# Kernel optimization log

Hardware: AMD Instinct MI355X
Metric: run time of the kernel (lower is better)

## Reference

```python
import jax, jax.numpy as jnp
import numpy as np

N_NODES = 100000

def _gcn_conv(x, W, b, src, dst, ew, num_nodes):
    # x: [N, Fin], W: [Fin, Fout], src/dst: [Etot], ew: [Etot]
    xw = x @ W                                   # [N, Fout]
    deg = jax.ops.segment_sum(ew, dst, num_segments=num_nodes)   # [N]
    dinv = jnp.where(deg > 0, jax.lax.rsqrt(jnp.where(deg > 0, deg, 1.0)), 0.0)
    norm = dinv[src] * ew * dinv[dst]            # [Etot]
    msg = xw[src] * norm[:, None]                # [Etot, Fout] gather-transform
    out = jax.ops.segment_sum(msg, dst, num_segments=num_nodes)  # scatter-add
    return out + b

def setup_inputs() -> dict:
    key = jax.random.key(0)
    k1, k2, k3, k4, k5, k6, k7 = jax.random.split(key, 7)
    N, E, F_IN, HID, CLS = N_NODES, 1600000, 128, 64, 32
    x = jax.random.normal(k1, (N, F_IN), dtype=jnp.float32)
    edge_index = jax.random.randint(k2, (2, E), 0, N, dtype=jnp.int64)
    edge_weight = jax.random.uniform(k3, (E,), dtype=jnp.float32)
    s1 = 1.0 / np.sqrt(F_IN)
    s2 = 1.0 / np.sqrt(HID)
    W1 = jax.random.uniform(k4, (F_IN, HID), dtype=jnp.float32, minval=-s1, maxval=s1)
    b1 = jnp.zeros((HID,), dtype=jnp.float32)
    W2 = jax.random.uniform(k5, (HID, CLS), dtype=jnp.float32, minval=-s2, maxval=s2)
    b2 = jnp.zeros((CLS,), dtype=jnp.float32)
    return {"x": x, "edge_index": edge_index, "edge_weight": edge_weight,
            "W1": W1, "b1": b1, "W2": W2, "b2": b2}

def reference(x, edge_index, edge_weight, W1, b1, W2, b2):
    N = x.shape[0]
    # add self-loops with weight 1 (PyG GCNConv default)
    loop = jnp.arange(N, dtype=edge_index.dtype)
    src = jnp.concatenate([edge_index[0], loop])
    dst = jnp.concatenate([edge_index[1], loop])
    ew = jnp.concatenate([edge_weight, jnp.ones((N,), dtype=edge_weight.dtype)])
    h = _gcn_conv(x, W1, b1, src, dst, ew, N)
    h = jax.nn.relu(h)
    # dropout is identity in eval mode
    out = _gcn_conv(h, W2, b2, src, dst, ew, N)
    return out
```

## Files before the change

### kernel.cpp

```cpp
#include <hip/hip_runtime.h>

#define FIN 128
#define HID 64
#define CLS 32

#define BSH 7
#define BNODES 128
#define GB 1024
#define BCAP 4096

using bfrag = __attribute__((ext_vector_type(8))) short;
using cfrag = __attribute__((ext_vector_type(4))) float;

__device__ inline unsigned short f2bf(float x) {
  unsigned u = __float_as_uint(x);
  return (unsigned short)((u + 0x7FFFu + ((u >> 16) & 1u)) >> 16);
}
__device__ inline void bf8_to_f32(int4 v, float* f) {
  f[0] = __uint_as_float((unsigned)v.x << 16);
  f[1] = __uint_as_float((unsigned)v.x & 0xFFFF0000u);
  f[2] = __uint_as_float((unsigned)v.y << 16);
  f[3] = __uint_as_float((unsigned)v.y & 0xFFFF0000u);
  f[4] = __uint_as_float((unsigned)v.z << 16);
  f[5] = __uint_as_float((unsigned)v.z & 0xFFFF0000u);
  f[6] = __uint_as_float((unsigned)v.w << 16);
  f[7] = __uint_as_float((unsigned)v.w & 0xFFFF0000u);
}

__global__ __launch_bounds__(256) void k_wpack(const float* __restrict__ W1,
                                               const float* __restrict__ W2,
                                               unsigned short* __restrict__ wp1,
                                               unsigned short* __restrict__ wp2) {
  int t = blockIdx.x * 256 + threadIdx.x;
  int total = gridDim.x * 256;
  for (int i = t; i < 16 * 512; i += total) {
    int f = i >> 9, l = (i >> 3) & 63, j = i & 7;
    int ks = f >> 2, nt = f & 3;
    int k = ks * 32 + (l >> 4) * 8 + j;
    int n = nt * 16 + (l & 15);
    wp1[i] = f2bf(W1[k * 64 + n]);
  }
  for (int i = t; i < 4 * 512; i += total) {
    int f = i >> 9, l = (i >> 3) & 63, j = i & 7;
    int ks = f >> 1, nt = f & 1;
    int k = ks * 32 + (l >> 4) * 8 + j;
    int n = nt * 16 + (l & 15);
    wp2[i] = f2bf(W2[k * 32 + n]);
  }
}

__global__ __launch_bounds__(256) void k_a1(const int* __restrict__ dst,
                                            int* __restrict__ gcntT,
                                            int E, int CHUNK, int NBUK) {
  __shared__ int cnt[1024];
  for (int i = threadIdx.x; i < NBUK; i += 256) cnt[i] = 0;
  __syncthreads();
  int s = blockIdx.x * CHUNK, e = min(E, s + CHUNK);
  for (int p = s + threadIdx.x; p < e; p += 256)
    atomicAdd(&cnt[dst[p] >> BSH], 1);
  __syncthreads();
  for (int i = threadIdx.x; i < NBUK; i += 256)
    gcntT[i * GB + blockIdx.x] = cnt[i];
}

__global__ __launch_bounds__(256) void k_scan_sums(const int* __restrict__ counts,
                                                   int* __restrict__ bsum, int N) {
  __shared__ int s[256];
  int base = blockIdx.x * 4096 + threadIdx.x * 16;
  int t = 0;
#pragma unroll
  for (int j = 0; j < 16; ++j)
    if (base + j < N) t += counts[base + j];
  s[threadIdx.x] = t;
  __syncthreads();
  for (int off = 128; off > 0; off >>= 1) {
    if (threadIdx.x < off) s[threadIdx.x] += s[threadIdx.x + off];
    __syncthreads();
  }
  if (threadIdx.x == 0) bsum[blockIdx.x] = s[0];
}

__global__ __launch_bounds__(256) void k_scan_bsums(int* __restrict__ bsum, int nb) {
  __shared__ int s[256];
  int t = threadIdx.x;
  int v = (t < nb) ? bsum[t] : 0;
  s[t] = v;
  __syncthreads();
  for (int off = 1; off < 256; off <<= 1) {
    int u = (t >= off) ? s[t - off] : 0;
    __syncthreads();
    s[t] += u;
    __syncthreads();
  }
  if (t < nb) bsum[t] = s[t] - v;
}

__global__ __launch_bounds__(256) void k_scan_emit(const int* __restrict__ counts,
                                                   const int* __restrict__ bsum,
                                                   int* __restrict__ rowstart, int N) {
  __shared__ int s[256];
  int base = blockIdx.x * 4096 + threadIdx.x * 16;
  int c[16];
  int tsum = 0;
#pragma unroll
  for (int j = 0; j < 16; ++j) {
    c[j] = (base + j < N) ? counts[base + j] : 0;
    tsum += c[j];
  }
  s[threadIdx.x] = tsum;
  __syncthreads();
  for (int off = 1; off < 256; off <<= 1) {
    int v = (threadIdx.x >= off) ? s[threadIdx.x - off] : 0;
    __syncthreads();
    s[threadIdx.x] += v;
    __syncthreads();
  }
  int run = bsum[blockIdx.x] + s[threadIdx.x] - tsum;
#pragma unroll
  for (int j = 0; j < 16; ++j) {
    if (base + j < N) rowstart[base + j] = run;
    run += c[j];
  }
}

__global__ __launch_bounds__(256) void k_a2(const int* __restrict__ src,
                                            const int* __restrict__ dst,
                                            const float* __restrict__ ew,
                                            const int* __restrict__ goff,
                                            int2* __restrict__ recs,
                                            int E, int CHUNK, int NBUK) {
  __shared__ int cur[1024];
  for (int i = threadIdx.x; i < NBUK; i += 256)
    cur[i] = goff[i * GB + blockIdx.x];
  __syncthreads();
  int s = blockIdx.x * CHUNK, e = min(E, s + CHUNK);
  for (int p = s + threadIdx.x; p < e; p += 256) {
    int d = dst[p];
    int b = d >> BSH;
    int pos = atomicAdd(&cur[b], 1);
    recs[pos] = make_int2(src[p] | ((d & (BNODES - 1)) << 17), __float_as_int(ew[p]));
  }
}

__global__ __launch_bounds__(256) void k_bucket(int2* __restrict__ recs,
                                                const int* __restrict__ goff,
                                                float* __restrict__ dinv,
                                                int* __restrict__ rowstart,
                                                int N, int E, int NBUK) {
  __shared__ int2 lrec[BCAP];
  __shared__ int cnt[BNODES];
  __shared__ int cur[BNODES];
  __shared__ int sbuf[BNODES];
  __shared__ float degs[BNODES];
  __shared__ float dl[BNODES];
  const int b = blockIdx.x;
  const int t = threadIdx.x;
  const int bstart = goff[b * GB];
  const int bend = (b + 1 < NBUK) ? goff[(b + 1) * GB] : E;
  int m = bend - bstart;
  if (m > BCAP) m = BCAP;

  if (t < BNODES) { cnt[t] = 0; degs[t] = 1.0f; }
  __syncthreads();
  for (int p = t; p < m; p += 256) {
    int2 r = recs[bstart + p];
    lrec[p] = r;
    int d = (r.x >> 17) & (BNODES - 1);
    atomicAdd(&cnt[d], 1);
    atomicAdd(&degs[d], __int_as_float(r.y));
  }
  __syncthreads();
  if (t < BNODES) sbuf[t] = cnt[t];
  __syncthreads();
  for (int off = 1; off < BNODES; off <<= 1) {
    int v = (t < BNODES && t >= off) ? sbuf[t - off] : 0;
    __syncthreads();
    if (t < BNODES) sbuf[t] += v;
    __syncthreads();
  }
  if (t < BNODES) {
    int ls = sbuf[t] - cnt[t];
    cur[t] = ls;
    float di = rsqrtf(degs[t]);
    dl[t] = di;
    int node = b * BNODES + t;
    if (node < N) { dinv[node] = di; rowstart[node] = bstart + ls; }
  }
  __syncthreads();
  for (int p = t; p < m; p += 256) {
    int2 r = lrec[p];
    int d = (r.x >> 17) & (BNODES - 1);
    int pos = atomicAdd(&cur[d], 1);
    float c = __int_as_float(r.y) * dl[d];
    recs[bstart + pos] = make_int2(r.x & 0x1FFFF, __float_as_int(c));
  }
}

template <int K, int F, bool RELU>
__global__ __launch_bounds__(256, 4) void mfma_gemm(const float* __restrict__ x,
                                                    const unsigned short* __restrict__ wp,
                                                    const float* __restrict__ scale,
                                                    unsigned short* __restrict__ y, int N) {
  constexpr int KS = K / 32;
  constexpr int NT = F / 16;
  const int lane = threadIdx.x & 63;
  const int quad = lane >> 4;
  const int col = lane & 15;
  const int row0 = blockIdx.x * 64 + (threadIdx.x >> 6) * 16;
  if (row0 >= N) return;

  bfrag bf[KS * NT];
#pragma unroll
  for (int f = 0; f < KS * NT; ++f)
    bf[f] = *(const bfrag*)(wp + f * 512 + lane * 8);

  cfrag acc[NT] = {};

  int row_a = row0 + col;
  if (row_a >= N) row_a = N - 1;
  const float* xp = x + (size_t)row_a * K + quad * 8;

#pragma unroll
  for (int ks = 0; ks < KS; ++ks) {
    float4 a0 = *(const float4*)(xp + ks * 32);
    float4 a1 = *(const float4*)(xp + ks * 32 + 4);
    if (RELU) {
      a0.x = fmaxf(a0.x, 0.f); a0.y = fmaxf(a0.y, 0.f);
      a0.z = fmaxf(a0.z, 0.f); a0.w = fmaxf(a0.w, 0.f);
      a1.x = fmaxf(a1.x, 0.f); a1.y = fmaxf(a1.y, 0.f);
      a1.z = fmaxf(a1.z, 0.f); a1.w = fmaxf(a1.w, 0.f);
    }
    bfrag af;
    af[0] = (short)f2bf(a0.x); af[1] = (short)f2bf(a0.y);
    af[2] = (short)f2bf(a0.z); af[3] = (short)f2bf(a0.w);
    af[4] = (short)f2bf(a1.x); af[5] = (short)f2bf(a1.y);
    af[6] = (short)f2bf(a1.z); af[7] = (short)f2bf(a1.w);
#pragma unroll
    for (int nt = 0; nt < NT; ++nt)
      acc[nt] = __builtin_amdgcn_mfma_f32_16x16x32_bf16(af, bf[ks * NT + nt], acc[nt], 0, 0, 0);
  }

  float scr[4];
#pragma unroll
  for (int r = 0; r < 4; ++r) {
    int row = row0 + quad * 4 + r;
    scr[r] = (row < N) ? scale[row] : 0.f;
  }
#pragma unroll
  for (int nt = 0; nt < NT; ++nt)
#pragma unroll
    for (int r = 0; r < 4; ++r) {
      int row = row0 + quad * 4 + r;
      if (row < N)
        y[(size_t)row * F + nt * 16 + col] = f2bf(scr[r] * acc[nt][r]);
    }
}

template <int F>
__global__ __launch_bounds__(256) void pull_agg(const unsigned short* __restrict__ xs,
                                                const int2* __restrict__ pairs,
                                                const int* __restrict__ rowstart,
                                                const float* __restrict__ dinv,
                                                const float* __restrict__ b,
                                                float* __restrict__ out, int N, int E) {
  constexpr int LPN = F / 8;
  constexpr int NPB = 256 / LPN;
  const int g = blockIdx.x * NPB + threadIdx.x / LPN;
  const int f8 = (threadIdx.x % LPN) * 8;
  if (g >= N) return;

  const int start = rowstart[g];
  const int end = (g + 1 < N) ? rowstart[g + 1] : E;
  const float di = dinv[g];

  float acc[8];
  {
    int4 v = *(const int4*)&xs[(size_t)g * F + f8];
    float xf[8];
    bf8_to_f32(v, xf);
    float4 b0 = *(const float4*)&b[f8];
    float4 b1 = *(const float4*)&b[f8 + 4];
    acc[0] = fmaf(di, xf[0], b0.x); acc[1] = fmaf(di, xf[1], b0.y);
    acc[2] = fmaf(di, xf[2], b0.z); acc[3] = fmaf(di, xf[3], b0.w);
    acc[4] = fmaf(di, xf[4], b1.x); acc[5] = fmaf(di, xf[5], b1.y);
    acc[6] = fmaf(di, xf[6], b1.z); acc[7] = fmaf(di, xf[7], b1.w);
  }

  int p = start;
  for (; p + 2 <= end; p += 2) {
    int2 p0 = pairs[p];
    int2 p1 = pairs[p + 1];
    int4 v0 = *(const int4*)&xs[(size_t)p0.x * F + f8];
    int4 v1 = *(const int4*)&xs[(size_t)p1.x * F + f8];
    float c0 = __int_as_float(p0.y), c1 = __int_as_float(p1.y);
    float x0[8], x1[8];
    bf8_to_f32(v0, x0);
    bf8_to_f32(v1, x1);
#pragma unroll
    for (int j = 0; j < 8; ++j) acc[j] = fmaf(c0, x0[j], acc[j]);
#pragma unroll
    for (int j = 0; j < 8; ++j) acc[j] = fmaf(c1, x1[j], acc[j]);
  }
  if (p < end) {
    int2 pa = pairs[p];
    int4 va = *(const int4*)&xs[(size_t)pa.x * F + f8];
    float ca = __int_as_float(pa.y);
    float xa[8];
    bf8_to_f32(va, xa);
#pragma unroll
    for (int j = 0; j < 8; ++j) acc[j] = fmaf(ca, xa[j], acc[j]);
  }
  *(float4*)&out[(size_t)g * F + f8] = make_float4(acc[0], acc[1], acc[2], acc[3]);
  *(float4*)&out[(size_t)g * F + f8 + 4] = make_float4(acc[4], acc[5], acc[6], acc[7]);
}

extern "C" void kernel_launch(void* const* d_in, const int* in_sizes, int n_in,
                              void* d_out, int out_size, void* d_ws, size_t ws_size,
                              hipStream_t stream) {
  const float* x  = (const float*)d_in[0];
  const int*   ei = (const int*)d_in[1];
  const float* ew = (const float*)d_in[2];
  const float* W1 = (const float*)d_in[3];
  const float* b1 = (const float*)d_in[4];
  const float* W2 = (const float*)d_in[5];
  const float* b2 = (const float*)d_in[6];
  float* out = (float*)d_out;

  const int N = in_sizes[0] / FIN;
  const int E = in_sizes[2];
  const int* src = ei;
  const int* dst = ei + E;

  const int NBUK = (N + BNODES - 1) >> BSH;
  const int M = NBUK * GB;
  const int CHUNK = (E + GB - 1) / GB;
  const int nbM = (M + 4095) / 4096;

  float* wsf      = (float*)d_ws;
  float* dinv     = wsf;
  int*   rowstart = (int*)(dinv + N);
  int*   gcntT    = rowstart + N;
  int*   bsum     = gcntT + M;
  int2*  recs     = (int2*)(bsum + 256);
  unsigned short* xs1 = (unsigned short*)(recs + E);
  float* out1     = (float*)(xs1 + (size_t)N * HID);
  unsigned short* xs2 = xs1;
  unsigned short* wp1 = (unsigned short*)(out1 + (size_t)N * HID);
  unsigned short* wp2 = wp1 + 16 * 512;

  k_wpack<<<32, 256, 0, stream>>>(W1, W2, wp1, wp2);
  k_a1<<<GB, 256, 0, stream>>>(dst, gcntT, E, CHUNK, NBUK);
  k_scan_sums<<<nbM, 256, 0, stream>>>(gcntT, bsum, M);
  k_scan_bsums<<<1, 256, 0, stream>>>(bsum, nbM);
  k_scan_emit<<<nbM, 256, 0, stream>>>(gcntT, bsum, gcntT, M);
  k_a2<<<GB, 256, 0, stream>>>(src, dst, ew, gcntT, recs, E, CHUNK, NBUK);
  k_bucket<<<NBUK, 256, 0, stream>>>(recs, gcntT, dinv, rowstart, N, E, NBUK);

  mfma_gemm<FIN, HID, false><<<(N + 63) / 64, 256, 0, stream>>>(x, wp1, dinv, xs1, N);
  pull_agg<HID><<<(N + 31) / 32, 256, 0, stream>>>(xs1, recs, rowstart, dinv, b1, out1, N, E);

  mfma_gemm<HID, CLS, true><<<(N + 63) / 64, 256, 0, stream>>>(out1, wp2, dinv, xs2, N);
  pull_agg<CLS><<<(N + 63) / 64, 256, 0, stream>>>(xs2, recs, rowstart, dinv, b2, out, N, E);
}
```

Baseline: 260.6 us.

## Stage edge records in LDS per block before coalesced bucket scatter

The record-scatter kernel now counts each bucket locally, prefix-scans the counts and writes records into a shared-memory staging buffer grouped by bucket. It then copies the staged records out in order, so consecutive threads write mostly contiguous runs of global memory instead of fully random positions. The grid block count GB drops from 1024 to 256, so each block handles a larger chunk (up to SCAP records). This adds an extra pass over dst, several barriers and about 70KB of LDS per block, which lowers occupancy. The serial per-bucket p2b fill loop may also be imbalanced.

```diff
diff --git a/kernel.cpp b/kernel.cpp
--- a/kernel.cpp
+++ b/kernel.cpp
@@ -6,8 +6,9 @@
 
 #define BSH 7
 #define BNODES 128
-#define GB 1024
+#define GB 256
 #define BCAP 4096
+#define SCAP 6272
 
 using bfrag = __attribute__((ext_vector_type(8))) short;
 using cfrag = __attribute__((ext_vector_type(4))) float;
@@ -129,16 +130,65 @@
                                             const int* __restrict__ goff,
                                             int2* __restrict__ recs,
                                             int E, int CHUNK, int NBUK) {
-  __shared__ int cur[1024];
-  for (int i = threadIdx.x; i < NBUK; i += 256)
-    cur[i] = goff[i * GB + blockIdx.x];
-  __syncthreads();
-  int s = blockIdx.x * CHUNK, e = min(E, s + CHUNK);
-  for (int p = s + threadIdx.x; p < e; p += 256) {
+  __shared__ int2 stage[SCAP];
+  __shared__ unsigned short p2b[SCAP];
+  __shared__ int lcnt[1024];
+  __shared__ int loff[1024];
+  __shared__ int lcur[1024];
+  __shared__ int gstart[1024];
+  __shared__ int ssum[256];
+  const int b = blockIdx.x, t = threadIdx.x;
+  const int s = b * CHUNK, e = min(E, s + CHUNK);
+  const int m = e - s;
+
+  for (int i = t; i < NBUK; i += 256) {
+    lcnt[i] = 0;
+    gstart[i] = goff[i * GB + b];
+  }
+  __syncthreads();
+  for (int p = s + t; p < e; p += 256)
+    atomicAdd(&lcnt[dst[p] >> BSH], 1);
+  __syncthreads();
+
+  int c[4];
+  int base = t * 4;
+  int tsum = 0;
+#pragma unroll
+  for (int j = 0; j < 4; ++j) {
+    c[j] = (base + j < NBUK) ? lcnt[base + j] : 0;
+    tsum += c[j];
+  }
+  ssum[t] = tsum;
+  __syncthreads();
+  for (int off = 1; off < 256; off <<= 1) {
+    int v = (t >= off) ? ssum[t - off] : 0;
+    __syncthreads();
+    ssum[t] += v;
+    __syncthreads();
+  }
+  int run = ssum[t] - tsum;
+#pragma unroll
+  for (int j = 0; j < 4; ++j) {
+    if (base + j < NBUK) { loff[base + j] = run; lcur[base + j] = run; }
+    run += c[j];
+  }
+  __syncthreads();
+
+  for (int i = t; i < NBUK; i += 256) {
+    int st = loff[i], en = st + lcnt[i];
+    for (int p = st; p < en; ++p) p2b[p] = (unsigned short)i;
+  }
+  for (int p = s + t; p < e; p += 256) {
     int d = dst[p];
-    int b = d >> BSH;
-    int pos = atomicAdd(&cur[b], 1);
-    recs[pos] = make_int2(src[p] | ((d & (BNODES - 1)) << 17), __float_as_int(ew[p]));
+    int bk = d >> BSH;
+    int pos = atomicAdd(&lcur[bk], 1);
+    stage[pos] = make_int2(src[p] | ((d & (BNODES - 1)) << 17), __float_as_int(ew[p]));
+  }
+  __syncthreads();
+
+  for (int p = t; p < m; p += 256) {
+    int bk = p2b[p];
+    recs[gstart[bk] + (p - loff[bk])] = stage[p];
   }
 }
 
```

New measurement: 254.6 us. 2.3% less time.

## Locally sort edge chunks in LDS before bucket scatter, staging output in shared

Applied to the files above, without the earlier changes.

Replaces the count pass plus global random scatter with a per-chunk LDS counting sort. It writes chunk-sorted records contiguously, along with per-chunk bucket offsets. The bucket kernel then gathers each bucket's contiguous segments from every chunk and writes the final CSR pairs coalesced from shared memory. This is meant to replace scattered global writes with coalesced ones and to read dst only within one kernel, at the cost of more LDS, an extra edge-sized buffer, and serial per-thread segment copies.

```diff
diff --git a/kernel.cpp b/kernel.cpp
--- a/kernel.cpp
+++ b/kernel.cpp
@@ -6,8 +6,10 @@
 
 #define BSH 7
 #define BNODES 128
-#define GB 1024
+#define GB 256
 #define BCAP 4096
+#define SCAP 6272
+#define NBUKP 800
 
 using bfrag = __attribute__((ext_vector_type(8))) short;
 using cfrag = __attribute__((ext_vector_type(4))) float;
@@ -49,18 +51,52 @@
   }
 }
 
-__global__ __launch_bounds__(256) void k_a1(const int* __restrict__ dst,
-                                            int* __restrict__ gcntT,
-                                            int E, int CHUNK, int NBUK) {
-  __shared__ int cnt[1024];
-  for (int i = threadIdx.x; i < NBUK; i += 256) cnt[i] = 0;
-  __syncthreads();
-  int s = blockIdx.x * CHUNK, e = min(E, s + CHUNK);
-  for (int p = s + threadIdx.x; p < e; p += 256)
-    atomicAdd(&cnt[dst[p] >> BSH], 1);
-  __syncthreads();
-  for (int i = threadIdx.x; i < NBUK; i += 256)
-    gcntT[i * GB + blockIdx.x] = cnt[i];
+__global__ __launch_bounds__(1024) void k_sortchunk(const int* __restrict__ src,
+                                                    const int* __restrict__ dst,
+                                                    const float* __restrict__ ew,
+                                                    int2* __restrict__ recsA,
+                                                    int* __restrict__ gcntT,
+                                                    int* __restrict__ loffB,
+                                                    int E, int CHUNK, int NBUK) {
+  __shared__ int2 stage[SCAP];
+  __shared__ int lcnt[NBUKP];
+  __shared__ int loff[NBUKP];
+  __shared__ int lcur[NBUKP];
+  __shared__ int ssum[1024];
+  const int b = blockIdx.x, t = threadIdx.x;
+  const int s = b * CHUNK, e = min(E, s + CHUNK);
+  const int m = e - s;
+
+  for (int i = t; i < NBUK; i += 1024) lcnt[i] = 0;
+  __syncthreads();
+  for (int p = s + t; p < e; p += 1024)
+    atomicAdd(&lcnt[dst[p] >> BSH], 1);
+  __syncthreads();
+
+  int c = (t < NBUK) ? lcnt[t] : 0;
+  ssum[t] = c;
+  __syncthreads();
+  for (int off = 1; off < 1024; off <<= 1) {
+    int v = (t >= off) ? ssum[t - off] : 0;
+    __syncthreads();
+    ssum[t] += v;
+    __syncthreads();
+  }
+  if (t < NBUK) { loff[t] = ssum[t] - c; lcur[t] = ssum[t] - c; }
+  if (t == 0) loff[NBUK] = m;
+  __syncthreads();
+
+  for (int p = s + t; p < e; p += 1024) {
+    int d = dst[p];
+    int bk = d >> BSH;
+    int pos = atomicAdd(&lcur[bk], 1);
+    stage[pos] = make_int2(src[p] | ((d & (BNODES - 1)) << 17), __float_as_int(ew[p]));
+  }
+  __syncthreads();
+
+  for (int p = t; p < m; p += 1024) recsA[s + p] = stage[p];
+  for (int i = t; i < NBUK; i += 1024) gcntT[i * GB + b] = lcnt[i];
+  for (int i = t; i <= NBUK; i += 1024) loffB[b * NBUKP + i] = loff[i];
 }
 
 __global__ __launch_bounds__(256) void k_scan_sums(const int* __restrict__ counts,
@@ -123,31 +159,15 @@
   }
 }
 
-__global__ __launch_bounds__(256) void k_a2(const int* __restrict__ src,
-                                            const int* __restrict__ dst,
-                                            const float* __restrict__ ew,
-                                            const int* __restrict__ goff,
-                                            int2* __restrict__ recs,
-                                            int E, int CHUNK, int NBUK) {
-  __shared__ int cur[1024];
-  for (int i = threadIdx.x; i < NBUK; i += 256)
-    cur[i] = goff[i * GB + blockIdx.x];
-  __syncthreads();
-  int s = blockIdx.x * CHUNK, e = min(E, s + CHUNK);
-  for (int p = s + threadIdx.x; p < e; p += 256) {
-    int d = dst[p];
-    int b = d >> BSH;
-    int pos = atomicAdd(&cur[b], 1);
-    recs[pos] = make_int2(src[p] | ((d & (BNODES - 1)) << 17), __float_as_int(ew[p]));
-  }
-}
-
-__global__ __launch_bounds__(256) void k_bucket(int2* __restrict__ recs,
+__global__ __launch_bounds__(256) void k_bucket(const int2* __restrict__ recsA,
                                                 const int* __restrict__ goff,
+                                                const int* __restrict__ loffB,
+                                                int2* __restrict__ pairs,
                                                 float* __restrict__ dinv,
                                                 int* __restrict__ rowstart,
-                                                int N, int E, int NBUK) {
+                                                int N, int E, int CHUNK, int NBUK) {
   __shared__ int2 lrec[BCAP];
+  __shared__ int2 sout[BCAP];
   __shared__ int cnt[BNODES];
   __shared__ int cur[BNODES];
   __shared__ int sbuf[BNODES];
@@ -162,9 +182,21 @@
 
   if (t < BNODES) { cnt[t] = 0; degs[t] = 1.0f; }
   __syncthreads();
+
+  {
+    int ls = loffB[t * NBUKP + b];
+    int le = loffB[t * NBUKP + b + 1];
+    int doff = goff[b * GB + t] - bstart;
+    const int2* sp = recsA + (size_t)t * CHUNK + ls;
+    int len = le - ls;
+    for (int j = 0; j < len; ++j) {
+      if (doff + j < BCAP) lrec[doff + j] = sp[j];
+    }
+  }
+  __syncthreads();
+
   for (int p = t; p < m; p += 256) {
-    int2 r = recs[bstart + p];
-    lrec[p] = r;
+    int2 r = lrec[p];
     int d = (r.x >> 17) & (BNODES - 1);
     atomicAdd(&cnt[d], 1);
     atomicAdd(&degs[d], __int_as_float(r.y));
@@ -192,8 +224,10 @@
     int d = (r.x >> 17) & (BNODES - 1);
     int pos = atomicAdd(&cur[d], 1);
     float c = __int_as_float(r.y) * dl[d];
-    recs[bstart + pos] = make_int2(r.x & 0x1FFFF, __float_as_int(c));
-  }
+    sout[pos] = make_int2(r.x & 0x1FFFF, __float_as_int(c));
+  }
+  __syncthreads();
+  for (int p = t; p < m; p += 256) pairs[bstart + p] = sout[p];
 }
 
 template <int K, int F, bool RELU>
@@ -340,25 +374,27 @@
   float* dinv     = wsf;
   int*   rowstart = (int*)(dinv + N);
   int*   gcntT    = rowstart + N;
-  int*   bsum     = gcntT + M;
-  int2*  recs     = (int2*)(bsum + 256);
-  unsigned short* xs1 = (unsigned short*)(recs + E);
+  int*   loffB    = gcntT + M;
+  int*   bsum     = loffB + GB * NBUKP;
+  int2*  recsA    = (int2*)(bsum + 256);
+  int2*  pairs    = recsA + E;
+  unsigned short* xs1 = (unsigned short*)(pairs + E);
   float* out1     = (float*)(xs1 + (size_t)N * HID);
   unsigned short* xs2 = xs1;
   unsigned short* wp1 = (unsigned short*)(out1 + (size_t)N * HID);
   unsigned short* wp2 = wp1 + 16 * 512;
 
   k_wpack<<<32, 256, 0, stream>>>(W1, W2, wp1, wp2);
-  k_a1<<<GB, 256, 0, stream>>>(dst, gcntT, E, CHUNK, NBUK);
+  k_sortchunk<<<GB, 1024, 0, stream>>>(src, dst, ew, recsA, gcntT, loffB, E, CHUNK, NBUK);
   k_scan_sums<<<nbM, 256, 0, stream>>>(gcntT, bsum, M);
   k_scan_bsums<<<1, 256, 0, stream>>>(bsum, nbM);
   k_scan_emit<<<nbM, 256, 0, stream>>>(gcntT, bsum, gcntT, M);
-  k_a2<<<GB, 256, 0, stream>>>(src, dst, ew, gcntT, recs, E, CHUNK, NBUK);
-  k_bucket<<<NBUK, 256, 0, stream>>>(recs, gcntT, dinv, rowstart, N, E, NBUK);
+  k_bucket<<<NBUK, 256, 0, stream>>>(recsA, gcntT, loffB, pairs, dinv, rowstart,
+                                     N, E, CHUNK, NBUK);
 
   mfma_gemm<FIN, HID, false><<<(N + 63) / 64, 256, 0, stream>>>(x, wp1, dinv, xs1, N);
-  pull_agg<HID><<<(N + 31) / 32, 256, 0, stream>>>(xs1, recs, rowstart, dinv, b1, out1, N, E);
+  pull_agg<HID><<<(N + 31) / 32, 256, 0, stream>>>(xs1, pairs, rowstart, dinv, b1, out1, N, E);
 
   mfma_gemm<HID, CLS, true><<<(N + 63) / 64, 256, 0, stream>>>(out1, wp2, dinv, xs2, N);
-  pull_agg<CLS><<<(N + 63) / 64, 256, 0, stream>>>(xs2, recs, rowstart, dinv, b2, out, N, E);
-}
+  pull_agg<CLS><<<(N + 63) / 64, 256, 0, stream>>>(xs2, pairs, rowstart, dinv, b2, out, N, E);
+}
```

Result: faster. 248.7 us (-4.6%).
